# Performance work log

Measured on AMD Instinct MI355X. Metric: run time of the kernel, lower is better.

The kernel has to match this reference:

```python
import jax, jax.numpy as jnp
import numpy as np

EMBED_DIM = 256
NUM_HEADS = 8


def setup_inputs() -> dict:
    key = jax.random.key(0)
    k1, k2, k3, k4 = jax.random.split(key, 4)
    b, nq, h, w = 2, 900, 16, 16
    attn_scores = jax.random.normal(k1, (b, nq, nq), dtype=jnp.float32)
    reference_points = jax.random.normal(k2, (b, nq, h, w), dtype=jnp.float32)
    # topology_proj = Linear(1, embed) -> ReLU -> Linear(embed, num_heads)
    w1 = jax.random.normal(k3, (EMBED_DIM,), dtype=jnp.float32) / 1.0  # Linear(1,E) weight, shape [E,1] squeezed
    b1 = jnp.zeros((EMBED_DIM,), dtype=jnp.float32)
    w2 = jax.random.normal(k4, (EMBED_DIM, NUM_HEADS), dtype=jnp.float32) / np.sqrt(EMBED_DIM)
    b2 = jnp.zeros((NUM_HEADS,), dtype=jnp.float32)
    lam = jnp.float32(0.1)
    return {"attn_scores": attn_scores, "reference_points": reference_points,
            "lam": lam, "w1": w1, "b1": b1, "w2": w2, "b2": b2}


def _process_reference_points(ref_pts):
    # ref_pts: [b, nq, h, w] -> argmax location normalized to [0,1]
    b, nq, h, w = ref_pts.shape
    flat = ref_pts.reshape(b, nq, h * w)
    idx = jnp.argmax(flat, axis=-1)                      # [b, nq] int
    y = (idx // w).astype(jnp.float32) / (h - 1)
    x = (idx % w).astype(jnp.float32) / (w - 1)
    return jnp.stack([x, y], axis=-1)                    # [b, nq, 2]


def reference(attn_scores, reference_points, lam, w1, b1, w2, b2):
    centers = _process_reference_points(reference_points)          # [b, nq, 2]
    # pairwise euclidean distance (torch.cdist)
    diff = centers[:, :, None, :] - centers[:, None, :, :]          # [b, nq, nq, 2]
    dist = jnp.sqrt(jnp.sum(diff * diff, axis=-1))                  # [b, nq, nq]
    mean_dist = jnp.mean(dist, axis=(1, 2), keepdims=True)
    topology = dist / (mean_dist + 1e-6)                            # [b, nq, nq]
    # tiny MLP on scalar feature: Linear(1,E) -> ReLU -> Linear(E,H)
    hdn = jax.nn.relu(topology[..., None] * w1 + b1)                # [b, nq, nq, E]
    bias = jnp.einsum('bqke,eh->bqkh', hdn, w2) + b2                # [b, nq, nq, H]
    bias_mean = jnp.mean(bias, axis=-1)                             # mean over heads -> [b, nq, nq]
    return attn_scores + lam * bias_mean
```

## Files before the change

### kernel.cpp

```cpp
#include <hip/hip_runtime.h>


#define NQ    900
#define LUT_N 451
#define TAG   0xC0DE0000u

__device__ __forceinline__ int aload_rlx(const int* p) {
    return __hip_atomic_load(p, __ATOMIC_RELAXED, __HIP_MEMORY_SCOPE_AGENT);
}
__device__ __forceinline__ void astore_rlx(int* p, int v) {
    __hip_atomic_store(p, v, __ATOMIC_RELAXED, __HIP_MEMORY_SCOPE_AGENT);
}

__global__ __launch_bounds__(256)
void k1_centers_stats(const float* __restrict__ ref,
                      const float* __restrict__ lam_p,
                      const float* __restrict__ w1,
                      const float* __restrict__ b1,
                      const float* __restrict__ w2,
                      const float* __restrict__ b2,
                      int* __restrict__ ws) {
    int*   cent2 = ws;
    float* lutg  = (float*)(ws + 900);

    const int tid  = threadIdx.x;
    const int lane = tid & 63;
    const int wave = tid >> 6;
    const int blk  = blockIdx.x;

    if (blk < 450) {
        __shared__ int ctmp[4];
        int q = blk * 4 + wave;
        const float* p = ref + (size_t)q * 256;
        float bv = p[lane];
        int   bi = lane;
        #pragma unroll
        for (int k = 1; k < 4; ++k) {
            float v = p[lane + 64 * k];
            if (v > bv) { bv = v; bi = lane + 64 * k; }
        }
        #pragma unroll
        for (int off = 32; off >= 1; off >>= 1) {
            float ov = __shfl_down(bv, off, 64);
            int   oi = __shfl_down(bi, off, 64);
            if (ov > bv || (ov == bv && oi < bi)) { bv = ov; bi = oi; }
        }
        if (lane == 0) ctmp[wave] = bi;
        __syncthreads();
        if (tid == 0) {
            int w0 = (int)(TAG | ((ctmp[0] & 255) << 8) | (ctmp[1] & 255));
            int w1v = (int)(TAG | ((ctmp[2] & 255) << 8) | (ctmp[3] & 255));
            astore_rlx(&cent2[blk * 2 + 0], w0);
            astore_rlx(&cent2[blk * 2 + 1], w1v);
        }
        return;
    }

    const int b = blk - 450;
    __shared__ int   idx_s[NQ];
    __shared__ float sqs[LUT_N];
    __shared__ int   hsh[256];
    __shared__ float w1s[256], b1s[256], wbars[256];
    __shared__ float wsum[4];

    hsh[tid] = 0;
    w1s[tid] = w1[tid];
    b1s[tid] = b1[tid];
    {
        float s8 = 0.f;
        #pragma unroll
        for (int h = 0; h < 8; ++h) s8 += w2[tid * 8 + h];
        wbars[tid] = s8 * 0.125f;
    }
    for (int s = tid; s < LUT_N; s += 256) sqs[s] = sqrtf((float)s);

    for (int k = tid; k < 450; k += 256) {
        int w;
        while (((unsigned)(w = aload_rlx(&cent2[b * 450 + k])) & 0xFFFF0000u) != TAG)
            __builtin_amdgcn_s_sleep(1);
        idx_s[2 * k]     = (w >> 8) & 255;
        idx_s[2 * k + 1] =  w       & 255;
    }
    __syncthreads();

    for (int k = tid; k < NQ; k += 256) atomicAdd(&hsh[idx_s[k]], 1);
    __syncthreads();

    float local = 0.f;
    {
        int h2v = hsh[tid];
        if (h2v) {
            int ix2 = tid & 15, iy2 = tid >> 4;
            for (int c1 = 0; c1 < 256; ++c1) {
                int h1 = hsh[c1];
                int dx = (c1 & 15) - ix2;
                int dy = (c1 >> 4) - iy2;
                local += (float)h1 * sqs[dx * dx + dy * dy];
            }
            local *= (float)h2v;
        }
    }
    #pragma unroll
    for (int off = 32; off >= 1; off >>= 1) local += __shfl_down(local, off, 64);
    if (lane == 0) wsum[wave] = local;
    __syncthreads();

    float tot   = wsum[0] + wsum[1] + wsum[2] + wsum[3];
    float mean  = tot * (1.f / 15.f) * (1.f / ((float)NQ * (float)NQ));
    float inv   = 1.f / (mean + 1e-6f);
    float b2bar = 0.125f * (b2[0] + b2[1] + b2[2] + b2[3] +
                            b2[4] + b2[5] + b2[6] + b2[7]);
    float lam   = lam_p[0];

    for (int s = tid; s < LUT_N; s += 256) {
        float t   = sqs[s] * (1.f / 15.f) * inv;
        float acc = b2bar;
        for (int i = 0; i < 256; ++i) {
            float hv = fmaf(t, w1s[i], b1s[i]);
            acc = fmaf(fmaxf(hv, 0.f), wbars[i], acc);
        }
        lutg[b * LUT_N + s] = lam * acc;
    }
}

__global__ __launch_bounds__(256)
void k2_apply(const float* __restrict__ attn,
              const int* __restrict__ ws,
              float* __restrict__ out) {
    const int* cent2 = ws;
    const float* lutg = (const float*)(ws + 900);
    int b = blockIdx.y;
    __shared__ float lut_s[LUT_N];
    __shared__ int   idx_s[NQ];
    for (int k = threadIdx.x; k < 450; k += 256) {
        int w = cent2[b * 450 + k];
        idx_s[2 * k]     = (w >> 8) & 255;
        idx_s[2 * k + 1] =  w       & 255;
    }
    for (int k = threadIdx.x; k < LUT_N; k += 256) lut_s[k] = lutg[b * LUT_N + k];
    __syncthreads();
    int t4 = blockIdx.x * 256 + threadIdx.x;
    if (t4 >= NQ * NQ / 4) return;
    int i  = t4 / 225;
    int j0 = (t4 - i * 225) * 4;
    int ci = idx_s[i];
    int ixi = ci & 15, iyi = ci >> 4;
    size_t base = (size_t)b * (NQ * NQ) + (size_t)i * NQ + j0;
    float4 a = *(const float4*)(attn + base);
    float r[4] = {a.x, a.y, a.z, a.w};
    #pragma unroll
    for (int u = 0; u < 4; ++u) {
        int cj = idx_s[j0 + u];
        int dx = ixi - (cj & 15), dy = iyi - (cj >> 4);
        r[u] += lut_s[dx * dx + dy * dy];
    }
    *(float4*)(out + base) = make_float4(r[0], r[1], r[2], r[3]);
}

extern "C" void kernel_launch(void* const* d_in, const int* in_sizes, int n_in,
                              void* d_out, int out_size, void* d_ws, size_t ws_size,
                              hipStream_t stream) {
    const float* attn = (const float*)d_in[0];
    const float* ref  = (const float*)d_in[1];
    const float* lam  = (const float*)d_in[2];
    const float* w1   = (const float*)d_in[3];
    const float* b1   = (const float*)d_in[4];
    const float* w2   = (const float*)d_in[5];
    const float* b2   = (const float*)d_in[6];
    float* out = (float*)d_out;
    int*   ws  = (int*)d_ws;

    k1_centers_stats<<<452, 256, 0, stream>>>(ref, lam, w1, b1, w2, b2, ws);
    k2_apply<<<dim3((NQ * NQ / 4 + 255) / 256, 2), 256, 0, stream>>>(attn, ws, out);
}
```

Before: 87.13 us.

## Split LUT build across two blocks per batch and pack centers for apply kernel

The stats kernel now launches two blocks per batch, and each builds half of the distance-to-bias lookup table, which halves the serial 256-step MLP loop per block. The first block also writes a compact 4-centers-per-int array. The apply kernel then loads only 225 ints instead of unpacking 450 words into 900 ints, and each thread handles four float4s, so 198 blocks per batch replace about 792. Each block does less setup, at the cost of more work per thread and fewer blocks in flight. The histogram and mean computation are still repeated in both stats blocks.

```diff
diff --git a/kernel.cpp b/kernel.cpp
--- a/kernel.cpp
+++ b/kernel.cpp
@@ -21,7 +21,8 @@
                       const float* __restrict__ b2,
                       int* __restrict__ ws) {
     int*   cent2 = ws;
-    float* lutg  = (float*)(ws + 900);
+    float* lutp  = (float*)(ws + 900);
+    int*   centp = ws + 900 + 2 * LUT_N;
 
     const int tid  = threadIdx.x;
     const int lane = tid & 63;
@@ -48,15 +49,16 @@
         if (lane == 0) ctmp[wave] = bi;
         __syncthreads();
         if (tid == 0) {
-            int w0 = (int)(TAG | ((ctmp[0] & 255) << 8) | (ctmp[1] & 255));
-            int w1v = (int)(TAG | ((ctmp[2] & 255) << 8) | (ctmp[3] & 255));
-            astore_rlx(&cent2[blk * 2 + 0], w0);
-            astore_rlx(&cent2[blk * 2 + 1], w1v);
+            astore_rlx(&cent2[blk*2+0], (int)(TAG | ((ctmp[0]&255)<<8) | (ctmp[1]&255)));
+            astore_rlx(&cent2[blk*2+1], (int)(TAG | ((ctmp[2]&255)<<8) | (ctmp[3]&255)));
         }
         return;
     }
 
-    const int b = blk - 450;
+    const int sb   = blk - 450;
+    const int b    = sb >> 1;
+    const int half = sb & 1;
+
     __shared__ int   idx_s[NQ];
     __shared__ float sqs[LUT_N];
     __shared__ int   hsh[256];
@@ -112,14 +114,25 @@
                             b2[4] + b2[5] + b2[6] + b2[7]);
     float lam   = lam_p[0];
 
-    for (int s = tid; s < LUT_N; s += 256) {
-        float t   = sqs[s] * (1.f / 15.f) * inv;
-        float acc = b2bar;
-        for (int i = 0; i < 256; ++i) {
-            float hv = fmaf(t, w1s[i], b1s[i]);
-            acc = fmaf(fmaxf(hv, 0.f), wbars[i], acc);
+    {
+        int s0  = half * 226;
+        int cnt = half ? 225 : 226;
+        if (tid < cnt) {
+            int   s   = s0 + tid;
+            float t   = sqs[s] * (1.f / 15.f) * inv;
+            float acc = b2bar;
+            for (int i = 0; i < 256; ++i) {
+                float hv = fmaf(t, w1s[i], b1s[i]);
+                acc = fmaf(fmaxf(hv, 0.f), wbars[i], acc);
+            }
+            lutp[b * LUT_N + s] = lam * acc;
         }
-        lutg[b * LUT_N + s] = lam * acc;
+    }
+    if (half == 0 && tid < 225) {
+        centp[b * 225 + tid] = (idx_s[4*tid] & 255) |
+                               ((idx_s[4*tid+1] & 255) << 8) |
+                               ((idx_s[4*tid+2] & 255) << 16) |
+                               ((idx_s[4*tid+3] & 255) << 24);
     }
 }
 
@@ -127,34 +140,36 @@
 void k2_apply(const float* __restrict__ attn,
               const int* __restrict__ ws,
               float* __restrict__ out) {
-    const int* cent2 = ws;
-    const float* lutg = (const float*)(ws + 900);
-    int b = blockIdx.y;
+    const float* lutp  = (const float*)(ws + 900);
+    const int*   centp = ws + 900 + 2 * LUT_N;
+    const int b = blockIdx.y;
+
     __shared__ float lut_s[LUT_N];
-    __shared__ int   idx_s[NQ];
-    for (int k = threadIdx.x; k < 450; k += 256) {
-        int w = cent2[b * 450 + k];
-        idx_s[2 * k]     = (w >> 8) & 255;
-        idx_s[2 * k + 1] =  w       & 255;
-    }
-    for (int k = threadIdx.x; k < LUT_N; k += 256) lut_s[k] = lutg[b * LUT_N + k];
+    __shared__ int   cpk[225];
+    if (threadIdx.x < 225) cpk[threadIdx.x] = centp[b * 225 + threadIdx.x];
+    for (int s = threadIdx.x; s < LUT_N; s += 256) lut_s[s] = lutp[b * LUT_N + s];
     __syncthreads();
-    int t4 = blockIdx.x * 256 + threadIdx.x;
-    if (t4 >= NQ * NQ / 4) return;
-    int i  = t4 / 225;
-    int j0 = (t4 - i * 225) * 4;
-    int ci = idx_s[i];
-    int ixi = ci & 15, iyi = ci >> 4;
-    size_t base = (size_t)b * (NQ * NQ) + (size_t)i * NQ + j0;
-    float4 a = *(const float4*)(attn + base);
-    float r[4] = {a.x, a.y, a.z, a.w};
+
+    const int base_f4 = blockIdx.x * 1024 + threadIdx.x;
     #pragma unroll
     for (int u = 0; u < 4; ++u) {
-        int cj = idx_s[j0 + u];
-        int dx = ixi - (cj & 15), dy = iyi - (cj >> 4);
-        r[u] += lut_s[dx * dx + dy * dy];
+        int f4 = base_f4 + u * 256;
+        if (f4 < 202500) {
+            int i  = f4 / 225;
+            int j4 = f4 - i * 225;
+            int ci = (cpk[i >> 2] >> ((i & 3) * 8)) & 255;
+            int ixi = ci & 15, iyi = ci >> 4;
+            int cw = cpk[j4];
+            size_t g = (size_t)b * (NQ * NQ) + (size_t)i * NQ + j4 * 4;
+            float4 a = *(const float4*)(attn + g);
+            int c, dx, dy;
+            c = cw & 255;         dx = ixi - (c & 15); dy = iyi - (c >> 4); a.x += lut_s[dx*dx + dy*dy];
+            c = (cw >> 8) & 255;  dx = ixi - (c & 15); dy = iyi - (c >> 4); a.y += lut_s[dx*dx + dy*dy];
+            c = (cw >> 16) & 255; dx = ixi - (c & 15); dy = iyi - (c >> 4); a.z += lut_s[dx*dx + dy*dy];
+            c = (cw >> 24) & 255; dx = ixi - (c & 15); dy = iyi - (c >> 4); a.w += lut_s[dx*dx + dy*dy];
+            *(float4*)(out + g) = a;
+        }
     }
-    *(float4*)(out + base) = make_float4(r[0], r[1], r[2], r[3]);
 }
 
 extern "C" void kernel_launch(void* const* d_in, const int* in_sizes, int n_in,
@@ -170,6 +185,6 @@
     float* out = (float*)d_out;
     int*   ws  = (int*)d_ws;
 
-    k1_centers_stats<<<452, 256, 0, stream>>>(ref, lam, w1, b1, w2, b2, ws);
-    k2_apply<<<dim3((NQ * NQ / 4 + 255) / 256, 2), 256, 0, stream>>>(attn, ws, out);
+    k1_centers_stats<<<454, 256, 0, stream>>>(ref, lam, w1, b1, w2, b2, ws);
+    k2_apply<<<dim3(198, 2), 256, 0, stream>>>(attn, ws, out);
 }
```

Measured after the change: 84.74 us. 2.7% less time.
